# Optimization experiments

Measured on AMD Instinct MI355X. Metric: run time of the kernel, lower is better.

## Reference

```python
import jax, jax.numpy as jnp
import numpy as np

D_MODEL = 512
HEADS = 8
D_K = D_MODEL // HEADS
D_FF = 2048
SEQ = 2048
BATCH = 8


def setup_inputs() -> dict:
    key = jax.random.key(0)
    ks = jax.random.split(key, 16)
    xavier = lambda k, shape: jax.random.uniform(
        k, shape, jnp.float32,
        -jnp.sqrt(6.0 / (shape[-2] + shape[-1])), jnp.sqrt(6.0 / (shape[-2] + shape[-1])))
    inp = {
        'x': jax.random.normal(ks[0], (SEQ, BATCH, D_MODEL), jnp.float32),
        'Wq': xavier(ks[1], (D_MODEL, D_MODEL)), 'bq': jnp.zeros((D_MODEL,)),
        'Wv': xavier(ks[2], (D_MODEL, D_MODEL)), 'bv': jnp.zeros((D_MODEL,)),
        'Wr': xavier(ks[3], (D_MODEL, D_MODEL)), 'br': jnp.zeros((D_MODEL,)),
        'W_h': xavier(ks[4], (HEADS, D_K, D_K)),
        'Wo': xavier(ks[5], (D_MODEL, D_MODEL)),
        'bo': jax.random.normal(ks[6], (D_MODEL,)) * 0.01,
        'ln1_g': jnp.ones((D_MODEL,)), 'ln1_b': jnp.zeros((D_MODEL,)),
        'Wf1': xavier(ks[7], (D_MODEL, D_FF)), 'bf1': jnp.zeros((D_FF,)),
        'Wf2': xavier(ks[8], (D_FF, D_MODEL)), 'bf2': jnp.zeros((D_MODEL,)),
        'ln2_g': jnp.ones((D_MODEL,)), 'ln2_b': jnp.zeros((D_MODEL,)),
    }
    return inp


def _layernorm(x, g, b, eps=1e-5):
    mu = jnp.mean(x, axis=-1, keepdims=True)
    var = jnp.var(x, axis=-1, keepdims=True)
    return (x - mu) * jax.lax.rsqrt(var + eps) * g + b


def _forward(x, Wq, bq, Wv, bv, Wr, br, W_h, Wo, bo, ln1_g, ln1_b, Wf1, bf1, Wf2, bf2, ln2_g, ln2_b):
    S, B, D = x.shape
    # causal mask: triu bool ADDED to scores (torch quirk: bool->float gives +1.0)
    mask = jnp.triu(jnp.ones((S, S), jnp.float32), k=1)
    xt = jnp.transpose(x, (1, 0, 2))  # (B, S, D)
    Q = (xt @ Wq.T + bq).reshape(B, S, HEADS, D_K).transpose(0, 2, 1, 3)  # bhsd
    V = (xt @ Wv.T + bv).reshape(B, S, HEADS, D_K).transpose(0, 2, 1, 3)
    Rp = (xt @ Wr.T + br).reshape(B, S, HEADS, D_K).transpose(0, 2, 1, 3)
    # recurrence: h_t = tanh(einsum('hnk,bhn->bhn', W_h, h) + R_t)
    # note: einsum sums W_h over k per (h,n) -> elementwise scale by W_h.sum(-1)
    w_diag = jnp.sum(W_h, axis=-1)  # (H, D_K)

    def step(h, r_t):
        h_new = jnp.tanh(h * w_diag + r_t)
        return h_new, h_new

    h0 = jnp.zeros((B, HEADS, D_K), x.dtype)
    _, H = jax.lax.scan(step, h0, jnp.transpose(Rp, (2, 0, 1, 3)))  # (S,B,H,Dk)
    H = jnp.transpose(H, (1, 2, 0, 3))  # (B,H,S,Dk)
    scale = 1.0 / np.sqrt(D_K)
    scores = jnp.einsum('bhqd,bhkd->bhqk', Q, H) * scale + mask
    attn = jax.nn.softmax(scores, axis=-1)
    out = jnp.einsum('bhqk,bhkd->bhqd', attn, V)
    out = out.transpose(0, 2, 1, 3).reshape(B, S, D)
    attn_out = out @ Wo.T + bo
    attn_out = jnp.transpose(attn_out, (1, 0, 2))  # back to (S,B,D)
    x1 = _layernorm(x + attn_out, ln1_g, ln1_b)
    ff = jax.nn.relu(x1 @ Wf1) + 0.0
    ff = (jax.nn.relu(x1 @ Wf1 + bf1)) @ Wf2 + bf2
    return _layernorm(x1 + ff, ln2_g, ln2_b)


def reference(x, Wq, bq, Wv, bv, Wr, br, W_h, Wo, bo, ln1_g, ln1_b, Wf1, bf1, Wf2, bf2, ln2_g, ln2_b):
    return _forward(x, Wq, bq, Wv, bv, Wr, br, W_h, Wo, bo, ln1_g, ln1_b, Wf1, bf1, Wf2, bf2, ln2_g, ln2_b)
```

## Files before the change

### kernel.cpp

```cpp
#include <hip/hip_runtime.h>
#include <hip/hip_bf16.h>
#include <math.h>

#define SEQ    2048
#define BATCH  8
#define DMODEL 512
#define NHEADS 8
#define DK     64
#define DFF    2048
#define MROWS  16384

typedef __hip_bfloat16 bf16;
typedef unsigned int   u32;
typedef unsigned short u16;
typedef __attribute__((ext_vector_type(8))) short short8;
typedef __attribute__((ext_vector_type(4))) float f32x4;

#define LOG2E  1.4426950408889634f
#define LOG2E2 2.8853900817779268f
#define MC2    1.4426950408889634f

__device__ __forceinline__ float b2f(bf16 v) { return __bfloat162float(v); }
__device__ __forceinline__ bf16  f2b(float f) { return __float2bfloat16(f); }
__device__ __forceinline__ u16 f2u(float f) { bf16 h = __float2bfloat16(f); return *(u16*)&h; }
__device__ __forceinline__ u32 pack2(float a, float b) {
    return ((u32)f2u(b) << 16) | (u32)f2u(a);
}
__device__ __forceinline__ void unpack2(u32 u, float& a, float& b) {
    a = __uint_as_float(u << 16);
    b = __uint_as_float(u & 0xFFFF0000u);
}
__device__ __forceinline__ float ldE(const void* p, long off, int f32) {
    return f32 ? ((const float*)p)[off] : b2f(((const bf16*)p)[off]);
}
__device__ __forceinline__ void async16(bf16* lds, const bf16* g) {
    __builtin_amdgcn_global_load_lds(
        (const __attribute__((address_space(1))) void*)g,
        (__attribute__((address_space(3))) void*)lds, 16, 0, 0);
}

__global__ __launch_bounds__(256) void probe_kernel(const void* __restrict__ x,
                                                    int* __restrict__ flag)
{
    int tid = threadIdx.x;
    const u16* u = (const u16*)x;
    int cnt = 0;
    #pragma unroll
    for (int i = 0; i < 8; i++) {
        u16 e = u[tid * 8 + i];
        float v = __uint_as_float(((u32)e) << 16);
        float a = fabsf(v);
        if (a > 9.313226e-10f && a < 1.0737418e9f) cnt++;
    }
    __shared__ int sh[256];
    sh[tid] = cnt;
    __syncthreads();
    for (int s = 128; s > 0; s >>= 1) {
        if (tid < s) sh[tid] += sh[tid + s];
        __syncthreads();
    }
    if (tid == 0) *flag = (sh[0] < 1700) ? 1 : 0;
}

__global__ __launch_bounds__(256) void prep_all(
    const void* x, bf16* __restrict__ xb,
    const void* Wq, const void* Wv, const void* Wr, const void* Wo,
    const void* Wf1, const void* Wf2,
    const void* bq, const void* bv, const void* br, const void* bo,
    const void* bf1, const void* bf2,
    bf16* __restrict__ Wqvr, bf16* __restrict__ Wob,
    bf16* __restrict__ Wf1t, bf16* __restrict__ Wf2t,
    bf16* __restrict__ bqvr, bf16* __restrict__ bob,
    bf16* __restrict__ bf1b, bf16* __restrict__ bf2b,
    const int* __restrict__ flagp)
{
    const int f32 = *flagp;
    int bid = blockIdx.x;
    if (bid < 4096) {
        int gid = bid * 256 + threadIdx.x;
        int row_in = gid >> 6;
        int d8 = (gid & 63) * 8;
        int s = row_in >> 3, b = row_in & 7;
        long src = (long)row_in * 512 + d8;
        long dst = ((long)b * SEQ + s) * 512 + d8;
        if (f32) {
            const float* xf = (const float*)x;
            float4 a = *(const float4*)(xf + src);
            float4 c = *(const float4*)(xf + src + 4);
            u32 o[4] = { pack2(a.x,a.y), pack2(a.z,a.w), pack2(c.x,c.y), pack2(c.z,c.w) };
            *(uint4*)(xb + dst) = *(uint4*)o;
        } else {
            *(uint4*)(xb + dst) = *(const uint4*)((const bf16*)x + src);
        }
        return;
    }
    long g = (long)(bid - 4096) * 256 + threadIdx.x;
    if (g < 786432) {
        if (g < 262144) Wqvr[g] = f2b(ldE(Wq, g, f32) * LOG2E);
        else if (g < 524288) Wqvr[g] = f2b(ldE(Wv, g & 262143, f32));
        else Wqvr[g] = f2b(ldE(Wr, g & 262143, f32));
    } else if (g < 1048576) {
        long j = g - 786432;
        Wob[j] = f2b(ldE(Wo, j, f32));
    } else if (g < 2097152) {
        long j = g - 1048576;
        long n = j >> 9, k = j & 511;
        Wf1t[j] = f2b(ldE(Wf1, k * 2048 + n, f32));
    } else if (g < 3145728) {
        long j = g - 2097152;
        long n = j >> 11, k = j & 2047;
        Wf2t[j] = f2b(ldE(Wf2, k * 512 + n, f32));
    } else {
        long j = g - 3145728;
        if (j < 512)       bqvr[j]      = f2b(ldE(bq, j, f32) * LOG2E);
        else if (j < 1024) bqvr[j]      = f2b(ldE(bv, j - 512, f32));
        else if (j < 1536) bqvr[j]      = f2b(ldE(br, j - 1024, f32));
        else if (j < 2048) bob[j-1536]  = f2b(ldE(bo, j - 1536, f32));
        else if (j < 4096) bf1b[j-2048] = f2b(ldE(bf1, j - 2048, f32));
        else if (j < 4608) bf2b[j-4096] = f2b(ldE(bf2, j - 4096, f32));
    }
}

template<bool RELU>
__device__ __forceinline__ void gemm_body(
    const bf16* __restrict__ A, const bf16* __restrict__ W,
    const bf16* __restrict__ bias, bf16* __restrict__ C,
    int K, int lda, int ldc, int bx, int by, bf16* As, bf16* Bs)
{
    const int tid = threadIdx.x;
    const int w = tid >> 6, lane = tid & 63;
    const int li = lane & 15, quad = lane >> 4;
    const int m0 = bx * 128, n0 = by * 128;
    const int wm = (w >> 1) * 64, wn = (w & 1) * 64;
    const int srow = lane >> 2, scol = (lane & 3) * 8;

    f32x4 acc[4][4];
    const f32x4 z4 = {0.f, 0.f, 0.f, 0.f};
    #pragma unroll
    for (int i = 0; i < 4; i++)
        #pragma unroll
        for (int j = 0; j < 4; j++) acc[i][j] = z4;

    const bf16* ga = A + (long)(m0 + w * 32 + srow) * lda + scol;
    const bf16* gb = W + (long)(n0 + w * 32 + srow) * K + scol;
    bf16* lA0 = &As[(w * 32) * 32];
    bf16* lA1 = &As[(w * 32 + 16) * 32];
    bf16* lB0 = &Bs[(w * 32) * 32];
    bf16* lB1 = &Bs[(w * 32 + 16) * 32];

    for (int k0 = 0; k0 < K; k0 += 64) {
        __syncthreads();
        async16(lA0, ga);
        async16(lA1, ga + (long)16 * lda);
        async16(lA0 + 4096, ga + 32);
        async16(lA1 + 4096, ga + 32 + (long)16 * lda);
        async16(lB0, gb);
        async16(lB1, gb + (long)16 * K);
        async16(lB0 + 4096, gb + 32);
        async16(lB1 + 4096, gb + 32 + (long)16 * K);
        ga += 64; gb += 64;
        __syncthreads();
        #pragma unroll
        for (int ks = 0; ks < 2; ks++) {
            short8 af[4], bfr[4];
            #pragma unroll
            for (int t = 0; t < 4; t++)
                af[t] = *(const short8*)&As[ks * 4096 + (wm + t * 16 + li) * 32 + quad * 8];
            #pragma unroll
            for (int t = 0; t < 4; t++)
                bfr[t] = *(const short8*)&Bs[ks * 4096 + (wn + t * 16 + li) * 32 + quad * 8];
            #pragma unroll
            for (int i = 0; i < 4; i++)
                #pragma unroll
                for (int j = 0; j < 4; j++)
                    acc[i][j] = __builtin_amdgcn_mfma_f32_16x16x32_bf16(
                        af[i], bfr[j], acc[i][j], 0, 0, 0);
        }
    }

    #pragma unroll
    for (int i = 0; i < 4; i++) {
        #pragma unroll
        for (int j = 0; j < 4; j++) {
            int col = n0 + wn + j * 16 + li;
            float bb = b2f(bias[col]);
            #pragma unroll
            for (int r = 0; r < 4; r++) {
                int row = m0 + wm + i * 16 + quad * 4 + r;
                float v = acc[i][j][r] + bb;
                if (RELU) v = fmaxf(v, 0.f);
                C[(long)row * ldc + col] = f2b(v);
            }
        }
    }
}

template<bool RELU>
__global__ __launch_bounds__(256) void mfma_gemm(
    const bf16* __restrict__ A, const bf16* __restrict__ W,
    const bf16* __restrict__ bias, bf16* __restrict__ C,
    int K, int lda, int ldc)
{
    __shared__ bf16 As[8192];
    __shared__ bf16 Bs[8192];
    gemm_body<RELU>(A, W, bias, C, K, lda, ldc, blockIdx.x, blockIdx.y, As, Bs);
}

__global__ __launch_bounds__(256) void recur_par(bf16* __restrict__ QVR,
                                                 const void* __restrict__ Wh,
                                                 const int* __restrict__ flagp)
{
    const int f32 = *flagp;
    const int idx = blockIdx.x * 256 + threadIdx.x;
    const int k   = idx >> 12;
    const int rem = idx & 4095;
    const int b   = rem >> 9, o = rem & 511;

    float w = 0.0f;
    #pragma unroll
    for (int j = 0; j < DK; j++) w += ldE(Wh, (long)o * DK + j, f32);
    const float w2 = w * LOG2E2;

    const bf16* rb = QVR + (long)b * SEQ * 1536 + 1024 + o;
    bf16*       hb = QVR + (long)b * SEQ * 1536 + 512  + o;

    const int s1   = k * 128;
    const int s0   = (k == 0) ? 0 : s1 - 64;
    const int warm = s1 - s0;
    const int TOT  = 128 + warm;

    const int PF = 32;
    float buf[PF];
    #pragma unroll
    for (int i = 0; i < PF; i++)
        buf[i] = b2f(rb[(long)(s0 + i) * 1536]) * LOG2E2;

    float h = 0.0f;
    for (int t = 0; t < TOT; t += PF) {
        float nbuf[PF];
        if (t + PF < TOT) {
            #pragma unroll
            for (int i = 0; i < PF; i++)
                nbuf[i] = b2f(rb[(long)(s0 + t + PF + i) * 1536]) * LOG2E2;
        }
        const bool store = (t >= warm);
        #pragma unroll
        for (int i = 0; i < PF; i++) {
            float xx = fmaf(h, w2, buf[i]);
            float e  = __builtin_amdgcn_exp2f(xx);
            float d  = __builtin_amdgcn_rcpf(e + 1.0f);
            h = fmaf(-2.0f, d, 1.0f);
            if (store) hb[(long)(s0 + t + i) * 1536] = f2b(h * 0.125f);
        }
        #pragma unroll
        for (int i = 0; i < PF; i++) buf[i] = nbuf[i];
    }
}

__global__ __launch_bounds__(256) void vt_kernel(const bf16* __restrict__ QVR,
                                                 bf16* __restrict__ VTg)
{
    __shared__ bf16 Ls[64 * 72];
    int bh = blockIdx.y, b = bh >> 3, h = bh & 7;
    int s0 = blockIdx.x * 64;
    int t = threadIdx.x;
    #pragma unroll
    for (int i = 0; i < 2; i++) {
        int item = t + i * 256;
        int s = item >> 3, d8 = (item & 7) * 8;
        uint4 v = *(const uint4*)&QVR[((long)(b * SEQ + s0 + s)) * 1536 + 512 + h * 64 + d8];
        *(uint2*)&Ls[s * 72 + d8]     = make_uint2(v.x, v.y);
        *(uint2*)&Ls[s * 72 + d8 + 4] = make_uint2(v.z, v.w);
    }
    __syncthreads();
    #pragma unroll
    for (int i = 0; i < 2; i++) {
        int item = t + i * 256;
        int d = item >> 3, sg = item & 7;
        bf16 tmp[8];
        #pragma unroll
        for (int j = 0; j < 8; j++) tmp[j] = Ls[(sg * 8 + j) * 72 + d];
        int sgp = (sg & 4) | ((sg & 3) ^ ((d >> 3) & 3));
        *(uint4*)&VTg[((long)bh * 64 + d) * 2048 + s0 + sgp * 8] = *(uint4*)tmp;
    }
}

__global__ __launch_bounds__(512) void attn_mfma(const bf16* __restrict__ QVR,
                                                 const bf16* __restrict__ VTg,
                                                 bf16* __restrict__ O)
{
    __shared__ bf16 Kt[2][4096];
    __shared__ bf16 Vt[2][4096];
    __shared__ bf16 Pl[8 * 32 * 40];
    const int tid = threadIdx.x;
    const int w = tid >> 6, lane = tid & 63;
    const int li = lane & 15, quad = lane >> 4;
    const int bh = blockIdx.y;
    const int b = bh >> 3, hd = bh & 7;
    const int q0 = blockIdx.x * 256;
    const int qw = q0 + w * 32;
    const long rowb = (long)b * SEQ;
    const bf16* Qb = QVR + hd * DK;
    const bf16* Hb = QVR + 512 + hd * DK;
    bf16* Pw = &Pl[w * 32 * 40];
    const f32x4 z4 = {0.f, 0.f, 0.f, 0.f};

    short8 ones;
    #pragma unroll
    for (int i = 0; i < 8; i++) ones[i] = (short)0x3F80;

    short8 qa[2][2];
    #pragma unroll
    for (int mt = 0; mt < 2; mt++)
        #pragma unroll
        for (int ks = 0; ks < 2; ks++)
            qa[mt][ks] = *(const short8*)&Qb[(rowb + qw + mt * 16 + li) * 1536
                                             + ks * 32 + quad * 8];

    f32x4 oacc[2][4];
    f32x4 lacc[2];
    #pragma unroll
    for (int mt = 0; mt < 2; mt++) {
        #pragma unroll
        for (int dt = 0; dt < 4; dt++) oacc[mt][dt] = z4;
        lacc[mt] = z4;
    }

    const bf16* gk = Hb + (rowb + w * 16 + (lane >> 2)) * 1536 + (lane & 3) * 8;
    const bf16* gv = VTg + ((long)bh * 64 + (w - 4) * 16 + (lane >> 2)) * 2048
                     + (lane & 3) * 8;

    if (w < 4) {
        async16(&Kt[0][w * 512],        gk);
        async16(&Kt[0][2048 + w * 512], gk + 32);
    } else {
        async16(&Vt[0][(w - 4) * 512],        gv);
        async16(&Vt[0][2048 + (w - 4) * 512], gv + 32);
    }
    gk += (long)64 * 1536;
    gv += 64;
    __syncthreads();

    for (int t = 0; t < 32; t++) {
        const int cb = t & 1, nb = cb ^ 1;

        if (t < 31) {
            if (w < 4) {
                async16(&Kt[nb][w * 512],        gk);
                async16(&Kt[nb][2048 + w * 512], gk + 32);
            } else {
                async16(&Vt[nb][(w - 4) * 512],        gv);
                async16(&Vt[nb][2048 + (w - 4) * 512], gv + 32);
            }
            gk += (long)64 * 1536;
            gv += 64;
        }

        const int kt2 = t * 64;
        const bf16* Kp = Kt[cb];
        const bf16* Vp = Vt[cb];

        #pragma unroll
        for (int half = 0; half < 2; half++) {
            const int kt2h = kt2 + half * 32;

            f32x4 sa[2][2];
            #pragma unroll
            for (int mt = 0; mt < 2; mt++)
                #pragma unroll
                for (int nt = 0; nt < 2; nt++) sa[mt][nt] = z4;
            #pragma unroll
            for (int ksd = 0; ksd < 2; ksd++) {
                short8 kb[2];
                #pragma unroll
                for (int nt = 0; nt < 2; nt++)
                    kb[nt] = *(const short8*)&Kp[ksd * 2048
                               + ((half * 2 + nt) * 16 + li) * 32 + quad * 8];
                #pragma unroll
                for (int mt = 0; mt < 2; mt++)
                    #pragma unroll
                    for (int nt = 0; nt < 2; nt++)
                        sa[mt][nt] = __builtin_amdgcn_mfma_f32_16x16x32_bf16(
                            qa[mt][ksd], kb[nt], sa[mt][nt], 0, 0, 0);
            }

            bool nomask  = (kt2h + 31 <= qw);
            bool allmask = (kt2h > qw + 31);
            if (nomask || allmask) {
                float MB = allmask ? MC2 : 0.0f;
                #pragma unroll
                for (int mt = 0; mt < 2; mt++)
                    #pragma unroll
                    for (int nt = 0; nt < 2; nt++) {
                        f32x4 s = sa[mt][nt];
                        #pragma unroll
                        for (int r = 0; r < 4; r++) {
                            float p = __builtin_amdgcn_exp2f(s[r] + MB);
                            Pw[(mt * 16 + quad * 4 + r) * 40 + nt * 16 + li] = f2b(p);
                        }
                    }
            } else {
                #pragma unroll
                for (int mt = 0; mt < 2; mt++) {
                    int qrow = qw + mt * 16 + quad * 4;
                    #pragma unroll
                    for (int nt = 0; nt < 2; nt++) {
                        int key = kt2h + nt * 16 + li;
                        f32x4 s = sa[mt][nt];
                        #pragma unroll
                        for (int r = 0; r < 4; r++) {
                            float arg = (key > qrow + r) ? s[r] + MC2 : s[r];
                            float p = __builtin_amdgcn_exp2f(arg);
                            Pw[(mt * 16 + quad * 4 + r) * 40 + nt * 16 + li] = f2b(p);
                        }
                    }
                }
            }

            short8 vbf[4], pa[2];
            #pragma unroll
            for (int dt = 0; dt < 4; dt++) {
                int d = dt * 16 + li;
                int sw = ((d >> 3) & 3) << 3;
                vbf[dt] = *(const short8*)&Vp[half * 2048 + d * 32 + ((quad * 8) ^ sw)];
            }
            #pragma unroll
            for (int mt = 0; mt < 2; mt++)
                pa[mt] = *(const short8*)&Pw[(mt * 16 + li) * 40 + quad * 8];
            #pragma unroll
            for (int mt = 0; mt < 2; mt++) {
                lacc[mt] = __builtin_amdgcn_mfma_f32_16x16x32_bf16(
                    pa[mt], ones, lacc[mt], 0, 0, 0);
                #pragma unroll
                for (int dt = 0; dt < 4; dt++)
                    oacc[mt][dt] = __builtin_amdgcn_mfma_f32_16x16x32_bf16(
                        pa[mt], vbf[dt], oacc[mt][dt], 0, 0, 0);
            }
        }

        __syncthreads();
    }

    #pragma unroll
    for (int mt = 0; mt < 2; mt++)
        #pragma unroll
        for (int r = 0; r < 4; r++) {
            float inv = 1.0f / lacc[mt][r];
            long row = rowb + qw + mt * 16 + quad * 4 + r;
            #pragma unroll
            for (int dt = 0; dt < 4; dt++)
                O[row * 512 + hd * 64 + dt * 16 + li] = f2b(oacc[mt][dt][r] * inv);
        }
}

__global__ __launch_bounds__(256) void ln1_kernel(const bf16* __restrict__ xb,
                                                  const bf16* __restrict__ ao,
                                                  const void* __restrict__ g,
                                                  const void* __restrict__ beta,
                                                  bf16* __restrict__ x1,
                                                  const int* __restrict__ flagp)
{
    const int f32 = *flagp;
    long base = (long)blockIdx.x * 512;
    int tid = threadIdx.x;
    int d2 = tid * 2;
    float x0, x1v, a0, a1;
    unpack2(*(const u32*)&xb[base + d2], x0, x1v);
    unpack2(*(const u32*)&ao[base + d2], a0, a1);
    float v0 = x0 + a0, v1 = x1v + a1;
    float s1 = v0 + v1;
    float s2 = v0 * v0 + v1 * v1;
    #pragma unroll
    for (int off = 32; off > 0; off >>= 1) {
        s1 += __shfl_down(s1, off);
        s2 += __shfl_down(s2, off);
    }
    __shared__ float w1[4], w2[4];
    int wid = tid >> 6, lane = tid & 63;
    if (lane == 0) { w1[wid] = s1; w2[wid] = s2; }
    __syncthreads();
    float t1 = w1[0] + w1[1] + w1[2] + w1[3];
    float t2 = w2[0] + w2[1] + w2[2] + w2[3];
    float mu = t1 * (1.0f / DMODEL);
    float var = t2 * (1.0f / DMODEL) - mu * mu;
    float rs = rsqrtf(var + 1e-5f);
    float r0 = (v0 - mu) * rs * ldE(g, d2, f32) + ldE(beta, d2, f32);
    float r1 = (v1 - mu) * rs * ldE(g, d2 + 1, f32) + ldE(beta, d2 + 1, f32);
    *(u32*)&x1[base + d2] = pack2(r0, r1);
}

__global__ __launch_bounds__(256) void ln2_kernel(const bf16* __restrict__ x1,
                                                  const bf16* __restrict__ ff2,
                                                  const void* __restrict__ g,
                                                  const void* __restrict__ beta,
                                                  void* __restrict__ outp,
                                                  const int* __restrict__ flagp)
{
    const int f32 = *flagp;
    int m = blockIdx.x;
    int b = m >> 11, s = m & 2047;
    long plain = (long)m * 512;
    long funny = ((long)s * BATCH + b) * 512;
    int tid = threadIdx.x;
    int d2 = tid * 2;
    float x0, x1v, a0, a1;
    unpack2(*(const u32*)&x1[plain + d2], x0, x1v);
    unpack2(*(const u32*)&ff2[plain + d2], a0, a1);
    float v0 = x0 + a0, v1 = x1v + a1;
    float s1 = v0 + v1;
    float s2 = v0 * v0 + v1 * v1;
    #pragma unroll
    for (int off = 32; off > 0; off >>= 1) {
        s1 += __shfl_down(s1, off);
        s2 += __shfl_down(s2, off);
    }
    __shared__ float w1[4], w2[4];
    int wid = tid >> 6, lane = tid & 63;
    if (lane == 0) { w1[wid] = s1; w2[wid] = s2; }
    __syncthreads();
    float t1 = w1[0] + w1[1] + w1[2] + w1[3];
    float t2 = w2[0] + w2[1] + w2[2] + w2[3];
    float mu = t1 * (1.0f / DMODEL);
    float var = t2 * (1.0f / DMODEL) - mu * mu;
    float rs = rsqrtf(var + 1e-5f);
    float r0 = (v0 - mu) * rs * ldE(g, d2, f32) + ldE(beta, d2, f32);
    float r1 = (v1 - mu) * rs * ldE(g, d2 + 1, f32) + ldE(beta, d2 + 1, f32);
    if (f32) {
        ((float*)outp)[funny + d2]     = r0;
        ((float*)outp)[funny + d2 + 1] = r1;
    } else {
        *(u32*)&((bf16*)outp)[funny + d2] = pack2(r0, r1);
    }
}

extern "C" void kernel_launch(void* const* d_in, const int* in_sizes, int n_in,
                              void* d_out, int out_size, void* d_ws, size_t ws_size,
                              hipStream_t stream)
{
    (void)in_sizes; (void)n_in; (void)out_size; (void)ws_size;
    const void* x = d_in[0];

    bf16* W    = (bf16*)d_ws;
    bf16* xb   = W;
    bf16* QVR  = W + (8u  << 20);
    bf16* Ob   = W + (32u << 20);
    bf16* VTg  = W + (40u << 20);
    bf16* AO   = W + (40u << 20);
    bf16* X1   = W + (8u  << 20);
    bf16* FFH  = W + (16u << 20);
    bf16* FF2  = W;
    int*  flag = (int*)((char*)d_ws + (size_t)96 * 1024 * 1024);
    bf16* Wt   = (bf16*)((char*)d_ws + (size_t)96 * 1024 * 1024 + 16);
    bf16* Wqvr = Wt;
    bf16* Wob  = Wt + 786432;
    bf16* Wf1t = Wt + 1048576;
    bf16* Wf2t = Wt + 2097152;
    bf16* bqvr = Wt + 3145728;
    bf16* bob  = Wt + 3147264;
    bf16* bf1b = Wt + 3147776;
    bf16* bf2b = Wt + 3149824;

    dim3 blk(256);
    probe_kernel<<<1, blk, 0, stream>>>(x, flag);
    prep_all<<<16402, blk, 0, stream>>>(
        x, xb,
        d_in[1], d_in[3], d_in[5], d_in[8], d_in[12], d_in[14],
        d_in[2], d_in[4], d_in[6], d_in[9], d_in[13], d_in[15],
        Wqvr, Wob, Wf1t, Wf2t, bqvr, bob, bf1b, bf2b, flag);

    mfma_gemm<false><<<dim3(128, 12), blk, 0, stream>>>(
        xb, Wqvr, bqvr, QVR, 512, 512, 1536);

    vt_kernel<<<dim3(32, 64), blk, 0, stream>>>(QVR, VTg);

    recur_par<<<256, blk, 0, stream>>>(QVR, d_in[7], flag);

    attn_mfma<<<dim3(8, 64), dim3(512), 0, stream>>>(QVR, VTg, Ob);

    mfma_gemm<false><<<dim3(128, 4), blk, 0, stream>>>(Ob, Wob, bob, AO, 512, 512, 512);

    ln1_kernel<<<MROWS, blk, 0, stream>>>(xb, AO, d_in[10], d_in[11], X1, flag);

    mfma_gemm<true><<<dim3(128, 16), blk, 0, stream>>>(X1, Wf1t, bf1b, FFH, 512, 512, 2048);

    mfma_gemm<false><<<dim3(128, 4), blk, 0, stream>>>(FFH, Wf2t, bf2b, FF2, 2048, 2048, 512);

    ln2_kernel<<<MROWS, blk, 0, stream>>>(X1, FF2, d_in[16], d_in[17], d_out, flag);
}
```

Measured before the change: 430.3 us.

## Swizzle K tile in attention LDS and use one wave per row in layernorms

The K tile loaded into shared memory in the attention kernel is now XOR-swizzled on its 16-byte chunks, and reads apply the matching XOR, to reduce LDS bank conflicts on the MFMA operand loads. Both layernorm kernels now give each 64-lane wave one 512-wide row, with 16-byte vector loads and stores and a wave-only xor-shuffle reduction. This drops the shared-memory reduction and the block barrier, and launches a quarter as many blocks. The swizzle has to match exactly between the async writes and the reads, or the results are wrong.

Result: slower. 470.4 us (+9.3%).

```diff
diff --git a/kernel.cpp b/kernel.cpp
--- a/kernel.cpp
+++ b/kernel.cpp
@@ -326,9 +326,11 @@
         lacc[mt] = z4;
     }
 
-    const bf16* gk = Hb + (rowb + w * 16 + (lane >> 2)) * 1536 + (lane & 3) * 8;
+    const bf16* gk = Hb + (rowb + w * 16 + (lane >> 2)) * 1536
+                     + (((lane & 3) ^ ((lane >> 3) & 3)) * 8);
     const bf16* gv = VTg + ((long)bh * 64 + (w - 4) * 16 + (lane >> 2)) * 2048
                      + (lane & 3) * 8;
+    const int gkr = (li >> 1) & 3;
 
     if (w < 4) {
         async16(&Kt[0][w * 512],        gk);
@@ -375,7 +377,8 @@
                 #pragma unroll
                 for (int nt = 0; nt < 2; nt++)
                     kb[nt] = *(const short8*)&Kp[ksd * 2048
-                               + ((half * 2 + nt) * 16 + li) * 32 + quad * 8];
+                               + ((half * 2 + nt) * 16 + li) * 32
+                               + ((quad ^ gkr) * 8)];
                 #pragma unroll
                 for (int mt = 0; mt < 2; mt++)
                     #pragma unroll
@@ -461,32 +464,43 @@
                                                   const int* __restrict__ flagp)
 {
     const int f32 = *flagp;
-    long base = (long)blockIdx.x * 512;
-    int tid = threadIdx.x;
-    int d2 = tid * 2;
-    float x0, x1v, a0, a1;
-    unpack2(*(const u32*)&xb[base + d2], x0, x1v);
-    unpack2(*(const u32*)&ao[base + d2], a0, a1);
-    float v0 = x0 + a0, v1 = x1v + a1;
-    float s1 = v0 + v1;
-    float s2 = v0 * v0 + v1 * v1;
+    const int w = threadIdx.x >> 6, lane = threadIdx.x & 63;
+    const long m = (long)blockIdx.x * 4 + w;
+    const long base = m * 512;
+    const int d0 = lane * 8;
+
+    uint4 xv = *(const uint4*)&xb[base + d0];
+    uint4 av = *(const uint4*)&ao[base + d0];
+    u32 xs[4] = { xv.x, xv.y, xv.z, xv.w };
+    u32 as[4] = { av.x, av.y, av.z, av.w };
+    float v[8];
+    float s1 = 0.f, s2 = 0.f;
+    #pragma unroll
+    for (int i = 0; i < 4; i++) {
+        float a0, a1, c0, c1;
+        unpack2(xs[i], a0, a1);
+        unpack2(as[i], c0, c1);
+        v[2*i]   = a0 + c0;
+        v[2*i+1] = a1 + c1;
+        s1 += v[2*i] + v[2*i+1];
+        s2 += v[2*i]*v[2*i] + v[2*i+1]*v[2*i+1];
+    }
     #pragma unroll
     for (int off = 32; off > 0; off >>= 1) {
-        s1 += __shfl_down(s1, off);
-        s2 += __shfl_down(s2, off);
-    }
-    __shared__ float w1[4], w2[4];
-    int wid = tid >> 6, lane = tid & 63;
-    if (lane == 0) { w1[wid] = s1; w2[wid] = s2; }
-    __syncthreads();
-    float t1 = w1[0] + w1[1] + w1[2] + w1[3];
-    float t2 = w2[0] + w2[1] + w2[2] + w2[3];
-    float mu = t1 * (1.0f / DMODEL);
-    float var = t2 * (1.0f / DMODEL) - mu * mu;
+        s1 += __shfl_xor(s1, off);
+        s2 += __shfl_xor(s2, off);
+    }
+    float mu = s1 * (1.0f / DMODEL);
+    float var = s2 * (1.0f / DMODEL) - mu * mu;
     float rs = rsqrtf(var + 1e-5f);
-    float r0 = (v0 - mu) * rs * ldE(g, d2, f32) + ldE(beta, d2, f32);
-    float r1 = (v1 - mu) * rs * ldE(g, d2 + 1, f32) + ldE(beta, d2 + 1, f32);
-    *(u32*)&x1[base + d2] = pack2(r0, r1);
+    u32 o[4];
+    #pragma unroll
+    for (int i = 0; i < 4; i++) {
+        float r0 = (v[2*i]   - mu) * rs * ldE(g, d0 + 2*i,     f32) + ldE(beta, d0 + 2*i,     f32);
+        float r1 = (v[2*i+1] - mu) * rs * ldE(g, d0 + 2*i + 1, f32) + ldE(beta, d0 + 2*i + 1, f32);
+        o[i] = pack2(r0, r1);
+    }
+    *(uint4*)&x1[base + d0] = *(uint4*)o;
 }
 
 __global__ __launch_bounds__(256) void ln2_kernel(const bf16* __restrict__ x1,
@@ -497,39 +511,52 @@
                                                   const int* __restrict__ flagp)
 {
     const int f32 = *flagp;
-    int m = blockIdx.x;
-    int b = m >> 11, s = m & 2047;
-    long plain = (long)m * 512;
-    long funny = ((long)s * BATCH + b) * 512;
-    int tid = threadIdx.x;
-    int d2 = tid * 2;
-    float x0, x1v, a0, a1;
-    unpack2(*(const u32*)&x1[plain + d2], x0, x1v);
-    unpack2(*(const u32*)&ff2[plain + d2], a0, a1);
-    float v0 = x0 + a0, v1 = x1v + a1;
-    float s1 = v0 + v1;
-    float s2 = v0 * v0 + v1 * v1;
+    const int w = threadIdx.x >> 6, lane = threadIdx.x & 63;
+    const int m = blockIdx.x * 4 + w;
+    const int b = m >> 11, s = m & 2047;
+    const long plain = (long)m * 512;
+    const long funny = ((long)s * BATCH + b) * 512;
+    const int d0 = lane * 8;
+
+    uint4 xv = *(const uint4*)&x1[plain + d0];
+    uint4 av = *(const uint4*)&ff2[plain + d0];
+    u32 xs[4] = { xv.x, xv.y, xv.z, xv.w };
+    u32 as[4] = { av.x, av.y, av.z, av.w };
+    float v[8];
+    float s1 = 0.f, s2 = 0.f;
+    #pragma unroll
+    for (int i = 0; i < 4; i++) {
+        float a0, a1, c0, c1;
+        unpack2(xs[i], a0, a1);
+        unpack2(as[i], c0, c1);
+        v[2*i]   = a0 + c0;
+        v[2*i+1] = a1 + c1;
+        s1 += v[2*i] + v[2*i+1];
+        s2 += v[2*i]*v[2*i] + v[2*i+1]*v[2*i+1];
+    }
     #pragma unroll
     for (int off = 32; off > 0; off >>= 1) {
-        s1 += __shfl_down(s1, off);
-        s2 += __shfl_down(s2, off);
-    }
-    __shared__ float w1[4], w2[4];
-    int wid = tid >> 6, lane = tid & 63;
-    if (lane == 0) { w1[wid] = s1; w2[wid] = s2; }
-    __syncthreads();
-    float t1 = w1[0] + w1[1] + w1[2] + w1[3];
-    float t2 = w2[0] + w2[1] + w2[2] + w2[3];
-    float mu = t1 * (1.0f / DMODEL);
-    float var = t2 * (1.0f / DMODEL) - mu * mu;
+        s1 += __shfl_xor(s1, off);
+        s2 += __shfl_xor(s2, off);
+    }
+    float mu = s1 * (1.0f / DMODEL);
+    float var = s2 * (1.0f / DMODEL) - mu * mu;
     float rs = rsqrtf(var + 1e-5f);
-    float r0 = (v0 - mu) * rs * ldE(g, d2, f32) + ldE(beta, d2, f32);
-    float r1 = (v1 - mu) * rs * ldE(g, d2 + 1, f32) + ldE(beta, d2 + 1, f32);
+    float r[8];
+    #pragma unroll
+    for (int i = 0; i < 8; i++)
+        r[i] = (v[i] - mu) * rs * ldE(g, d0 + i, f32) + ldE(beta, d0 + i, f32);
     if (f32) {
-        ((float*)outp)[funny + d2]     = r0;
-        ((float*)outp)[funny + d2 + 1] = r1;
+        float* op = (float*)outp + funny + d0;
+        float4 f0 = { r[0], r[1], r[2], r[3] };
+        float4 f1 = { r[4], r[5], r[6], r[7] };
+        *(float4*)(op)     = f0;
+        *(float4*)(op + 4) = f1;
     } else {
-        *(u32*)&((bf16*)outp)[funny + d2] = pack2(r0, r1);
+        u32 o[4];
+        #pragma unroll
+        for (int i = 0; i < 4; i++) o[i] = pack2(r[2*i], r[2*i+1]);
+        *(uint4*)&((bf16*)outp)[funny + d0] = *(uint4*)o;
     }
 }
 
@@ -579,11 +606,11 @@
 
     mfma_gemm<false><<<dim3(128, 4), blk, 0, stream>>>(Ob, Wob, bob, AO, 512, 512, 512);
 
-    ln1_kernel<<<MROWS, blk, 0, stream>>>(xb, AO, d_in[10], d_in[11], X1, flag);
+    ln1_kernel<<<MROWS / 4, blk, 0, stream>>>(xb, AO, d_in[10], d_in[11], X1, flag);
 
     mfma_gemm<true><<<dim3(128, 16), blk, 0, stream>>>(X1, Wf1t, bf1b, FFH, 512, 512, 2048);
 
     mfma_gemm<false><<<dim3(128, 4), blk, 0, stream>>>(FFH, Wf2t, bf2b, FF2, 2048, 2048, 512);
 
-    ln2_kernel<<<MROWS, blk, 0, stream>>>(X1, FF2, d_in[16], d_in[17], d_out, flag);
-}
+    ln2_kernel<<<MROWS / 4, blk, 0, stream>>>(X1, FF2, d_in[16], d_in[17], d_out, flag);
+}
```
